# Optimization experiments

Measured on AMD Instinct MI355X. Metric: run time of the kernel, lower is better.

## Reference

```python
import jax, jax.numpy as jnp
import numpy as np

N_USERS = 50000
N_ITEMS = 30000
N_ENT = 100000
N_REL = 11          # relations are 1..10; table has N_REL-1 rows
E = 500000          # KG triplets
EI = 1000000        # user-item interaction edges
D = 64              # emb_size (must equal 2*KD for router input)
KD = 32             # FactSemanticEmbedding embedding_dim (complex half-dim)
HID = 64            # GatingRouter hidden (channel)
HOPS = 3            # context_hops
NTH = 3             # hop_threshold N
GAMMA = 0.2


def setup_inputs() -> dict:
    key = jax.random.key(0)
    ks = jax.random.split(key, 24)
    g = lambda i, shape, s=0.1: (jax.random.normal(ks[i], shape) * s).astype(jnp.float32)
    return dict(
        user_embed=g(0, (N_USERS, D)), item_embed=g(1, (N_ITEMS, D)),
        Wq=g(2, (D, D)), Wk=g(3, (D, D)), Wv=g(4, (D, D)),
        ent_real=g(5, (N_ENT, KD)), ent_imag=g(6, (N_ENT, KD)),
        rel_real=g(7, (N_REL - 1, KD)), rel_imag=g(8, (N_REL - 1, KD)),
        fp_W1=g(9, (6 * KD, 2 * KD)), fp_b1=jnp.zeros((2 * KD,), jnp.float32),
        fp_W2=g(10, (2 * KD, 3)), fp_b2=jnp.zeros((3,), jnp.float32),
        rt_W1=g(11, (D, HID)), rt_b1=jnp.zeros((HID,), jnp.float32),
        rt_W2=g(12, (HID, D)), rt_b2=jnp.zeros((D,), jnp.float32),
        relation_emb=g(13, (N_REL - 1, D)),
        user_emb=g(14, (N_USERS, D)), entity_emb=g(15, (N_ENT, D)),
        inter_edge_w=jax.random.uniform(ks[16], (EI,), jnp.float32),
        edge_index=jax.random.randint(ks[17], (2, E), 0, N_ENT),
        edge_type=jax.random.randint(ks[18], (E,), 1, N_REL),
        inter_edge=jnp.stack([jax.random.randint(ks[19], (EI,), 0, N_USERS),
                              jax.random.randint(ks[20], (EI,), 0, N_ITEMS)]),
    )


def _normalize(x):  # F.normalize(dim=-1, eps=1e-8)
    n = jnp.linalg.norm(x, axis=-1, keepdims=True)
    return x / jnp.maximum(n, 1e-8)


def _n2n(x):
    return jnp.nan_to_num(x, nan=0.0, posinf=1e4, neginf=1e-4)


def reference(user_embed, item_embed, Wq, Wk, Wv, ent_real, ent_imag, rel_real,
              rel_imag, fp_W1, fp_b1, fp_W2, fp_b2, rt_W1, rt_b1, rt_W2, rt_b2,
              relation_emb, user_emb, entity_emb, inter_edge_w,
              edge_index, edge_type, inter_edge):
    users, items = inter_edge[0], inter_edge[1]
    # --- AttentionPreferenceMiner (dropout off / eval) ---
    q = (user_embed @ Wq)[users]           # [EI, D]
    k = (item_embed @ Wk)[items]
    v = (item_embed @ Wv)[items]
    scores = (q * k).sum(-1) / jnp.sqrt(jnp.float32(D)) * inter_edge_w
    m = jax.ops.segment_max(scores, users, num_segments=N_USERS)
    ex = jnp.exp(scores - m[users])
    den = jax.ops.segment_sum(ex, users, num_segments=N_USERS)
    alpha = ex / den[users]                # scatter_softmax over users
    cnt_u = jax.ops.segment_sum(jnp.ones_like(scores), users, num_segments=N_USERS)
    user_pref = jax.ops.segment_sum(v * alpha[:, None], users, num_segments=N_USERS)
    user_pref = user_pref / jnp.maximum(cnt_u, 1.0)[:, None]   # scatter_mean
    # --- FactSemanticEmbedding ---
    h, t = edge_index[0], edge_index[1]
    r = edge_type - 1
    hr, hi = ent_real[h], ent_imag[h]
    rr, ri = rel_real[r], rel_imag[r]
    tr, ti = ent_real[t], ent_imag[t]
    feat = jnp.concatenate([hr, hi, rr, ri, tr, ti], axis=-1)  # [E, 6*KD]
    w = jax.nn.softmax(jax.nn.sigmoid(feat @ fp_W1 + fp_b1) @ fp_W2 + fp_b2, axis=-1)
    br = w[:, 0:1] * hr + w[:, 1:2] * rr + w[:, 2:3] * tr
    bi = w[:, 0:1] * hi + w[:, 1:2] * ri + w[:, 2:3] * ti
    fact = jnp.concatenate([br, bi], axis=1)                   # [E, D]
    # --- GatingRouter: sum_j (aligned @ pref^T)[i,j] == aligned @ pref.sum(0) ---
    aligned = jax.nn.sigmoid(fact @ rt_W1 + rt_b1) @ rt_W2 + rt_b2
    omega = (aligned @ user_pref.sum(0)) / jnp.sqrt(jnp.float32(HID))  # [E]
    # --- GraphConv (mess_dropout off) ---
    rel_e = relation_emb[r]                                    # [E, D]
    cnt_h = jax.ops.segment_sum(jnp.ones((E,), omega.dtype), h, num_segments=N_ENT)
    seg_o = jax.ops.segment_sum(omega, h, num_segments=E)      # dim_size=omega.shape[0]
    alpha_g = omega / (seg_o[h] + 1e-8)
    eta = jnp.where(alpha_g > GAMMA, alpha_g, 0.0)
    seg_e = jax.ops.segment_sum(eta, h, num_segments=E)
    eta = eta / (seg_e[h] + 1e-8)
    e_emb, u_emb = entity_emb, user_emb
    ent_res, usr_res = entity_emb, user_emb
    for hop in range(1, HOPS + 1):
        neigh = e_emb[t] * rel_e
        rho = alpha_g if hop < NTH else eta
        e_agg = jax.ops.segment_sum(rho[:, None] * neigh, h, num_segments=N_ENT)
        e_agg = e_agg / jnp.maximum(cnt_h, 1.0)[:, None]       # scatter_mean
        item_agg = inter_edge_w[:, None] * e_emb[items]
        u_agg = jax.ops.segment_sum(item_agg, users, num_segments=N_USERS)
        e_emb = _n2n(_normalize(e_agg))
        u_emb = _n2n(_normalize(u_agg))
        ent_res = ent_res + e_emb
        usr_res = usr_res + u_emb
    return jnp.concatenate([ent_res, usr_res], axis=0)        # [N_ENT+N_USERS, D]
```

## Files before the change

### kernel.cpp

```cpp
#include <hip/hip_runtime.h>
#include <hip/hip_bf16.h>
#include <math.h>

#define N_USERS 50000
#define N_ITEMS 30000
#define N_ENT   100000
#define NE      500000
#define NEI     1000000
#define D       64
#define GAMMA   0.2f
#define LDP     65

#define UBK ((N_USERS + 255) / 256)
#define HBK ((N_ENT + 255) / 256)
#define PCHUNK 4096

typedef __hip_bfloat16 bf16;

__device__ __forceinline__ float wave_sum(float v) {
    #pragma unroll
    for (int off = 32; off > 0; off >>= 1) v += __shfl_xor(v, off, 64);
    return v;
}

__device__ __forceinline__ float g16_sum(float v) {
    #pragma unroll
    for (int off = 1; off < 16; off <<= 1) v += __shfl_xor(v, off, 64);
    return v;
}

__device__ __forceinline__ float bits2f(unsigned short u) {
    return __uint_as_float(((unsigned)u) << 16);
}

__device__ __forceinline__ unsigned short f2bf_bits(float f) {
    bf16 b = __float2bfloat16(f);
    return *(unsigned short*)&b;
}

__device__ __forceinline__ float sigmoidf(float x) {
    return __fdividef(1.0f, 1.0f + __expf(-x));
}

__device__ __forceinline__ float n2n(float y) {
    if (isnan(y)) return 0.0f;
    if (isinf(y)) return y > 0.0f ? 1e4f : 1e-4f;
    return y;
}

__global__ __launch_bounds__(256) void k_histb(const int* __restrict__ ie,
        const int* __restrict__ eidx, int* __restrict__ bcntU,
        int* __restrict__ bcntH, int UCH) {
    __shared__ int lc[HBK + 1];
    int t = threadIdx.x;
    int b = blockIdx.x;
    for (int i = t; i < HBK + 1; i += 256) lc[i] = 0;
    __syncthreads();
    if (b < UCH) {
        int base = b * PCHUNK;
        #pragma unroll
        for (int i = 0; i < PCHUNK / 256; i++) {
            int e = base + i * 256 + t;
            if (e < NEI) atomicAdd(&lc[ie[e] >> 8], 1);
        }
        __syncthreads();
        for (int i = t; i < UBK; i += 256) if (lc[i]) atomicAdd(&bcntU[i], lc[i]);
    } else {
        int base = (b - UCH) * PCHUNK;
        #pragma unroll
        for (int i = 0; i < PCHUNK / 256; i++) {
            int e = base + i * 256 + t;
            if (e < NE) atomicAdd(&lc[eidx[e] >> 8], 1);
        }
        __syncthreads();
        for (int i = t; i < HBK; i += 256) if (lc[i]) atomicAdd(&bcntH[i], lc[i]);
    }
}

__global__ void k_scanb(const int* __restrict__ bcntU, int* __restrict__ bOffU,
                        int* __restrict__ bcurU, const int* __restrict__ bcntH,
                        int* __restrict__ bOffH, int* __restrict__ bcurH,
                        int* __restrict__ offU, int* __restrict__ offH) {
    __shared__ int sh[512];
    int t = threadIdx.x;
    const int* c; int* o; int* cu; int n; int tot;
    if (blockIdx.x == 0) { c = bcntU; o = bOffU; cu = bcurU; n = UBK; tot = NEI; }
    else                 { c = bcntH; o = bOffH; cu = bcurH; n = HBK; tot = NE; }
    int v = (t < n) ? c[t] : 0;
    sh[t] = v;
    __syncthreads();
    for (int d = 1; d < 512; d <<= 1) {
        int x = (t >= d) ? sh[t - d] : 0;
        __syncthreads();
        sh[t] += x;
        __syncthreads();
    }
    if (t < n) { int ex = sh[t] - v; o[t] = ex; cu[t] = ex; }
    if (t == 0) {
        o[n] = tot;
        if (blockIdx.x == 0) offU[N_USERS] = NEI;
        else                 offH[N_ENT] = NE;
    }
}

__global__ __launch_bounds__(256) void k_part1(const int* __restrict__ ie,
        const float* __restrict__ w, const int* __restrict__ eidx,
        const int* __restrict__ etype, int* __restrict__ bcurU,
        int* __restrict__ bcurH, int2* __restrict__ stIW,
        int* __restrict__ stTR, int UCH) {
    __shared__ int lcnt[HBK + 1];
    __shared__ int lbase[HBK + 1];
    int t = threadIdx.x;
    int b = blockIdx.x;
    for (int i = t; i < HBK + 1; i += 256) lcnt[i] = 0;
    __syncthreads();
    if (b < UCH) {
        int base = b * PCHUNK;
        int bkt[PCHUNK / 256], rnk[PCHUNK / 256];
        #pragma unroll
        for (int i = 0; i < PCHUNK / 256; i++) {
            int e = base + i * 256 + t;
            bkt[i] = -1;
            rnk[i] = 0;
            if (e < NEI) {
                int k = ie[e] >> 8;
                bkt[i] = k;
                rnk[i] = atomicAdd(&lcnt[k], 1);
            }
        }
        __syncthreads();
        for (int i = t; i < UBK; i += 256)
            if (lcnt[i] > 0) lbase[i] = atomicAdd(&bcurU[i], lcnt[i]);
        __syncthreads();
        #pragma unroll
        for (int i = 0; i < PCHUNK / 256; i++) {
            int e = base + i * 256 + t;
            if (bkt[i] >= 0) {
                int pos = lbase[bkt[i]] + rnk[i];
                int ul = ie[e] & 255;
                stIW[pos] = make_int2(ie[NEI + e] | (ul << 24), __float_as_int(w[e]));
            }
        }
    } else {
        int base = (b - UCH) * PCHUNK;
        int bkt[PCHUNK / 256], rnk[PCHUNK / 256];
        #pragma unroll
        for (int i = 0; i < PCHUNK / 256; i++) {
            int e = base + i * 256 + t;
            bkt[i] = -1;
            rnk[i] = 0;
            if (e < NE) {
                int k = eidx[e] >> 8;
                bkt[i] = k;
                rnk[i] = atomicAdd(&lcnt[k], 1);
            }
        }
        __syncthreads();
        for (int i = t; i < HBK; i += 256)
            if (lcnt[i] > 0) lbase[i] = atomicAdd(&bcurH[i], lcnt[i]);
        __syncthreads();
        #pragma unroll
        for (int i = 0; i < PCHUNK / 256; i++) {
            int e = base + i * 256 + t;
            if (bkt[i] >= 0) {
                int pos = lbase[bkt[i]] + rnk[i];
                int hl = eidx[e] & 255;
                stTR[pos] = eidx[NE + e] | ((etype[e] - 1) << 20) | (hl << 24);
            }
        }
    }
}

__global__ __launch_bounds__(256) void k_part2(const int* __restrict__ bOffU,
        const int2* __restrict__ stIW, int* __restrict__ offU,
        int2* __restrict__ csr_itw, const int* __restrict__ bOffH,
        const int* __restrict__ stTR, int* __restrict__ offH,
        int2* __restrict__ csr_th, int UBKc) {
    __shared__ int lcnt[256];
    __shared__ int lcur[256];
    int t = threadIdx.x;
    int b = blockIdx.x;
    lcnt[t] = 0;
    __syncthreads();
    if (b < UBKc) {
        int s = bOffU[b], e = bOffU[b + 1];
        for (int j = s + t; j < e; j += 256)
            atomicAdd(&lcnt[((unsigned)stIW[j].x) >> 24], 1);
        __syncthreads();
        int v = lcnt[t];
        lcur[t] = v;
        __syncthreads();
        for (int d = 1; d < 256; d <<= 1) {
            int x = (t >= d) ? lcur[t - d] : 0;
            __syncthreads();
            lcur[t] += x;
            __syncthreads();
        }
        int base = s + lcur[t] - v;
        int u = (b << 8) + t;
        if (u < N_USERS) offU[u] = base;
        __syncthreads();
        lcur[t] = base;
        __syncthreads();
        for (int j = s + t; j < e; j += 256) {
            int2 r = stIW[j];
            int pos = atomicAdd(&lcur[((unsigned)r.x) >> 24], 1);
            csr_itw[pos] = make_int2(r.x & 0x00FFFFFF, r.y);
        }
    } else {
        int bb = b - UBKc;
        int s = bOffH[bb], e = bOffH[bb + 1];
        for (int j = s + t; j < e; j += 256)
            atomicAdd(&lcnt[((unsigned)stTR[j]) >> 24], 1);
        __syncthreads();
        int v = lcnt[t];
        lcur[t] = v;
        __syncthreads();
        for (int d = 1; d < 256; d <<= 1) {
            int x = (t >= d) ? lcur[t - d] : 0;
            __syncthreads();
            lcur[t] += x;
            __syncthreads();
        }
        int base = s + lcur[t] - v;
        int h = (bb << 8) + t;
        if (h < N_ENT) offH[h] = base;
        __syncthreads();
        lcur[t] = base;
        __syncthreads();
        for (int j = s + t; j < e; j += 256) {
            int r = stTR[j];
            int pos = atomicAdd(&lcur[((unsigned)r) >> 24], 1);
            csr_th[pos] = make_int2(r & 0x00FFFFFF,
                                    (bb << 8) + (int)(((unsigned)r) >> 24));
        }
    }
}

__device__ __forceinline__ void stage_rows2(const float* __restrict__ s0,
                                            const float* __restrict__ s1,
                                            float* At, int row0, int n, int t) {
    #pragma unroll
    for (int half = 0; half < 2; half++) {
        const float* src = half ? s1 : s0;
        int kofs = half ? 32 : 0;
        #pragma unroll
        for (int fi = t, it = 0; it < 2; fi += 256, it++) {
            int row = fi >> 3;
            int k4 = (fi & 7) << 2;
            float4 v = make_float4(0.f, 0.f, 0.f, 0.f);
            if (row0 + row < n) v = *(const float4*)&src[(size_t)(row0 + row) * 32 + k4];
            At[(kofs + k4 + 0) * LDP + row] = v.x;
            At[(kofs + k4 + 1) * LDP + row] = v.y;
            At[(kofs + k4 + 2) * LDP + row] = v.z;
            At[(kofs + k4 + 3) * LDP + row] = v.w;
        }
    }
}

__device__ __forceinline__ void stage_rows1(const float* __restrict__ src,
                                            float* At, int row0, int n, int t) {
    #pragma unroll
    for (int fi = t, it = 0; it < 4; fi += 256, it++) {
        int row = fi >> 4;
        int k4 = (fi & 15) << 2;
        float4 v = make_float4(0.f, 0.f, 0.f, 0.f);
        if (row0 + row < n) v = *(const float4*)&src[(size_t)(row0 + row) * 64 + k4];
        At[(k4 + 0) * LDP + row] = v.x;
        At[(k4 + 1) * LDP + row] = v.y;
        At[(k4 + 2) * LDP + row] = v.z;
        At[(k4 + 3) * LDP + row] = v.w;
    }
}

__global__ __launch_bounds__(256) void k_proj(const float* __restrict__ I,
        const float* __restrict__ Wk, const float* __restrict__ Wv,
        const float* __restrict__ UE, const float* __restrict__ Wq,
        bf16* __restrict__ IkB, float* __restrict__ Iv, float* __restrict__ Uq, int IB) {
    __shared__ float At[64 * LDP];
    int t = threadIdx.x;
    int b = blockIdx.x;
    int lane = t & 63;
    int wv = __builtin_amdgcn_readfirstlane(t >> 6);
    if (b < IB) {
        int row0 = b << 6;
        stage_rows1(I, At, row0, N_ITEMS, t);
        __syncthreads();
        const float* Wb = ((wv >> 1) ? Wv : Wk) + (wv & 1) * 32;
        float acc[32];
        #pragma unroll
        for (int c = 0; c < 32; c++) acc[c] = 0.f;
        for (int k = 0; k < 64; k++) {
            float a = At[k * LDP + lane];
            const float* wr = Wb + k * 64;
            #pragma unroll
            for (int c4 = 0; c4 < 8; c4++) {
                float4 w4 = *(const float4*)&wr[c4 * 4];
                acc[c4 * 4 + 0] += a * w4.x;
                acc[c4 * 4 + 1] += a * w4.y;
                acc[c4 * 4 + 2] += a * w4.z;
                acc[c4 * 4 + 3] += a * w4.w;
            }
        }
        int row = row0 + lane;
        if (row < N_ITEMS) {
            if (wv >> 1) {
                float* dst = Iv + (size_t)row * 64 + (wv & 1) * 32;
                #pragma unroll
                for (int c4 = 0; c4 < 8; c4++)
                    *(float4*)&dst[c4 * 4] = make_float4(acc[c4*4], acc[c4*4+1], acc[c4*4+2], acc[c4*4+3]);
            } else {
                bf16* dst = IkB + (size_t)row * 64 + (wv & 1) * 32;
                #pragma unroll
                for (int c4 = 0; c4 < 8; c4++) {
                    ushort4 s;
                    s.x = f2bf_bits(acc[c4 * 4 + 0]);
                    s.y = f2bf_bits(acc[c4 * 4 + 1]);
                    s.z = f2bf_bits(acc[c4 * 4 + 2]);
                    s.w = f2bf_bits(acc[c4 * 4 + 3]);
                    *(ushort4*)&dst[c4 * 4] = s;
                }
            }
        }
    } else {
        int row0 = (b - IB) << 6;
        stage_rows1(UE, At, row0, N_USERS, t);
        __syncthreads();
        const float* Wb = Wq + wv * 16;
        float acc[16];
        #pragma unroll
        for (int c = 0; c < 16; c++) acc[c] = 0.f;
        for (int k = 0; k < 64; k++) {
            float a = At[k * LDP + lane];
            const float* wr = Wb + k * 64;
            #pragma unroll
            for (int c4 = 0; c4 < 4; c4++) {
                float4 w4 = *(const float4*)&wr[c4 * 4];
                acc[c4 * 4 + 0] += a * w4.x;
                acc[c4 * 4 + 1] += a * w4.y;
                acc[c4 * 4 + 2] += a * w4.z;
                acc[c4 * 4 + 3] += a * w4.w;
            }
        }
        int row = row0 + lane;
        if (row < N_USERS) {
            float* dst = Uq + (size_t)row * 64 + wv * 16;
            #pragma unroll
            for (int c4 = 0; c4 < 4; c4++)
                *(float4*)&dst[c4 * 4] = make_float4(acc[c4*4], acc[c4*4+1], acc[c4*4+2], acc[c4*4+3]);
        }
    }
}

__global__ __launch_bounds__(256) void k_userAB(const int* __restrict__ offU,
                        const int2* __restrict__ itw,
                        const float* __restrict__ Uq, const bf16* __restrict__ IkB,
                        float* __restrict__ exA, float* __restrict__ c, int n) {
    int u = (blockIdx.x * blockDim.x + threadIdx.x) >> 6;
    int lane = threadIdx.x & 63;
    if (u >= n) return;
    int s = offU[u], e = offU[u + 1];
    if (s == e) return;
    int l = lane & 15, g = lane >> 4;
    float4 qv = *(const float4*)&Uq[(size_t)u * D + l * 4];
    const char* kbase = (const char*)IkB;
    unsigned dby = (unsigned)(l << 3);
    float den = 0.f;
    for (int j0 = s; j0 < e; j0 += 8) {
        int jA = j0 + g, jB = jA + 4;
        bool vA = jA < e, vB = jB < e;
        int2 iA = itw[vA ? jA : s];
        int2 iB = itw[vB ? jB : s];
        ushort4 kA = *(const ushort4*)(kbase + (((unsigned)iA.x) << 7) + dby);
        ushort4 kB = *(const ushort4*)(kbase + (((unsigned)iB.x) << 7) + dby);
        float dA = qv.x * bits2f(kA.x) + qv.y * bits2f(kA.y) +
                   qv.z * bits2f(kA.z) + qv.w * bits2f(kA.w);
        float dB = qv.x * bits2f(kB.x) + qv.y * bits2f(kB.y) +
                   qv.z * bits2f(kB.z) + qv.w * bits2f(kB.w);
        #pragma unroll
        for (int off = 1; off < 16; off <<= 1) {
            dA += __shfl_xor(dA, off, 64);
            dB += __shfl_xor(dB, off, 64);
        }
        float eAv = vA ? __expf(dA * 0.125f * __int_as_float(iA.y)) : 0.f;
        float eBv = vB ? __expf(dB * 0.125f * __int_as_float(iB.y)) : 0.f;
        den += eAv + eBv;
        if (vA && l == 0) exA[jA] = eAv;
        if (vB && l == 0) exA[jB] = eBv;
    }
    den += __shfl_xor(den, 16, 64);
    den += __shfl_xor(den, 32, 64);
    float inv = __fdividef(1.0f, den * (float)(e - s));
    asm volatile("s_waitcnt vmcnt(0)" ::: "memory");
    for (int j = s + lane; j < e; j += 64)
        atomicAdd(&c[itw[j].x], exA[j] * inv);
}

__global__ void k_pdense(const float* __restrict__ c, const float* __restrict__ Iv,
                         float* __restrict__ p, int n) {
    int lane = threadIdx.x & 63;
    int gw = blockIdx.x * 4 + (threadIdx.x >> 6);
    int nw = gridDim.x * 4;
    float acc = 0.f;
    for (int i = gw; i < n; i += nw) acc += c[i] * Iv[(size_t)i * D + lane];
    __shared__ float red[256];
    red[threadIdx.x] = acc;
    __syncthreads();
    if (threadIdx.x < 64) {
        float s = red[threadIdx.x] + red[threadIdx.x + 64] + red[threadIdx.x + 128] + red[threadIdx.x + 192];
        atomicAdd(&p[threadIdx.x], s);
    }
}

__global__ __launch_bounds__(256) void k_entabx(const float* __restrict__ er,
        const float* __restrict__ ei, const float* __restrict__ fpW1,
        const float* __restrict__ rr, const float* __restrict__ ri,
        const float* __restrict__ rtW1, const float* __restrict__ rtW2,
        const float* __restrict__ rt_b2, const float* __restrict__ p,
        float* __restrict__ EH, float* __restrict__ ET, float* __restrict__ PHI,
        float* __restrict__ RR1, float* __restrict__ PSI,
        float* __restrict__ v2, float* __restrict__ cb, int EB) {
    __shared__ float At[64 * LDP];
    int b = blockIdx.x;
    int t = threadIdx.x;
    if (b < EB) {
        int row0 = b << 6;
        stage_rows2(er, ei, At, row0, N_ENT, t);
        __syncthreads();
        int lane = t & 63;
        int wv = __builtin_amdgcn_readfirstlane(t >> 6);
        int row = row0 + lane;
        const float* Wb1 = fpW1 + ((wv >> 1) ? (128 * 64) : 0) + (wv & 1) * 32;
        const float* Wb2 = rtW1 + wv * 16;
        float acc[32];
        float acp[16];
        #pragma unroll
        for (int c = 0; c < 32; c++) acc[c] = 0.f;
        #pragma unroll
        for (int c = 0; c < 16; c++) acp[c] = 0.f;
        for (int k = 0; k < 64; k++) {
            float a = At[k * LDP + lane];
            const float* wr1 = Wb1 + k * 64;
            const float* wr2 = Wb2 + k * 64;
            #pragma unroll
            for (int c4 = 0; c4 < 8; c4++) {
                float4 w4 = *(const float4*)&wr1[c4 * 4];
                acc[c4 * 4 + 0] += a * w4.x;
                acc[c4 * 4 + 1] += a * w4.y;
                acc[c4 * 4 + 2] += a * w4.z;
                acc[c4 * 4 + 3] += a * w4.w;
            }
            #pragma unroll
            for (int c4 = 0; c4 < 4; c4++) {
                float4 w4 = *(const float4*)&wr2[c4 * 4];
                acp[c4 * 4 + 0] += a * w4.x;
                acp[c4 * 4 + 1] += a * w4.y;
                acp[c4 * 4 + 2] += a * w4.z;
                acp[c4 * 4 + 3] += a * w4.w;
            }
        }
        if (row < N_ENT) {
            float* dst = ((wv >> 1) ? ET : EH) + (size_t)row * 64 + (wv & 1) * 32;
            #pragma unroll
            for (int c4 = 0; c4 < 8; c4++)
                *(float4*)&dst[c4 * 4] = make_float4(acc[c4*4], acc[c4*4+1], acc[c4*4+2], acc[c4*4+3]);
            float* dsp = PHI + (size_t)row * 64 + wv * 16;
            #pragma unroll
            for (int c4 = 0; c4 < 4; c4++)
                *(float4*)&dsp[c4 * 4] = make_float4(acp[c4*4], acp[c4*4+1], acp[c4*4+2], acp[c4*4+3]);
        }
    } else if (b == EB) {
        if (t < 64) {
            int lane = t;
            for (int r = 0; r < 10; r++) {
                float a = 0.f, bb = 0.f;
                for (int k = 0; k < 32; k++) {
                    float sr = rr[r * 32 + k], si = ri[r * 32 + k];
                    a  += sr * fpW1[(64 + k) * D + lane] + si * fpW1[(96 + k) * D + lane];
                    bb += sr * rtW1[k * D + lane] + si * rtW1[(32 + k) * D + lane];
                }
                RR1[r * D + lane] = a;
                PSI[r * D + lane] = bb;
            }
        }
    } else {
        if (t < 64) {
            int j = t;
            float acc = 0.f;
            #pragma unroll
            for (int k = 0; k < D; k++) acc += rtW2[j * D + k] * p[k];
            v2[j] = acc;
            float cc = rt_b2[j] * p[j];
            cc = wave_sum(cc);
            if (j == 0) cb[0] = cc;
        }
    }
}

__global__ __launch_bounds__(256) void k_omegaE(const int2* __restrict__ csr_th,
                          const float* __restrict__ EH, const float* __restrict__ ET,
                          const float* __restrict__ PHI, const float* __restrict__ PSI,
                          const float* __restrict__ RR1, const float* __restrict__ fp_b1,
                          const float* __restrict__ fpW2, const float* __restrict__ fp_b2,
                          const float* __restrict__ rt_b1, const float* __restrict__ v2,
                          const float* __restrict__ cb, float* __restrict__ omg,
                          const float* __restrict__ src_emb, bf16* __restrict__ eA,
                          int NB) {
    int b = blockIdx.x;
    if (b >= NB) {
        int base = (b - NB) * 1024 + threadIdx.x * 4;
        float4 v = *(const float4*)&src_emb[base];
        ushort4 s;
        s.x = f2bf_bits(v.x); s.y = f2bf_bits(v.y);
        s.z = f2bf_bits(v.z); s.w = f2bf_bits(v.w);
        *(ushort4*)&eA[base] = s;
        return;
    }
    int grp = threadIdx.x >> 4;
    int l = threadIdx.x & 15;
    int d0 = l * 4;
    int jA = b * 32 + grp;
    int jB = jA + 16;
    float4 b1 = *(const float4*)&fp_b1[d0];
    float4 rb = *(const float4*)&rt_b1[d0];
    float4 vv = *(const float4*)&v2[d0];
    float cc = cb[0];
    float f0[4], f1[4], f2[4];
    #pragma unroll
    for (int c4 = 0; c4 < 4; c4++) {
        f0[c4] = fpW2[(d0 + c4) * 3 + 0];
        f1[c4] = fpW2[(d0 + c4) * 3 + 1];
        f2[c4] = fpW2[(d0 + c4) * 3 + 2];
    }
    float b20 = fp_b2[0], b21 = fp_b2[1], b22 = fp_b2[2];
    int2 thA = csr_th[jA];
    int2 thB = csr_th[jB];
    int tA = thA.x & 0xFFFFF, rA = thA.x >> 20, hA = thA.y;
    int tB = thB.x & 0xFFFFF, rB = thB.x >> 20, hB = thB.y;
    float4 ehA = *(const float4*)&EH[(size_t)hA * D + d0];
    float4 ehB = *(const float4*)&EH[(size_t)hB * D + d0];
    float4 phA = *(const float4*)&PHI[(size_t)hA * D + d0];
    float4 phB = *(const float4*)&PHI[(size_t)hB * D + d0];
    float4 etA = *(const float4*)&ET[(size_t)tA * D + d0];
    float4 etB = *(const float4*)&ET[(size_t)tB * D + d0];
    float4 ptA = *(const float4*)&PHI[(size_t)tA * D + d0];
    float4 ptB = *(const float4*)&PHI[(size_t)tB * D + d0];
    float4 rrA = *(const float4*)&RR1[rA * D + d0];
    float4 rrB = *(const float4*)&RR1[rB * D + d0];
    float4 psA = *(const float4*)&PSI[rA * D + d0];
    float4 psB = *(const float4*)&PSI[rB * D + d0];
    ehA.x += b1.x; ehA.y += b1.y; ehA.z += b1.z; ehA.w += b1.w;
    ehB.x += b1.x; ehB.y += b1.y; ehB.z += b1.z; ehB.w += b1.w;
    float zA0 = sigmoidf(ehA.x + rrA.x + etA.x);
    float zA1 = sigmoidf(ehA.y + rrA.y + etA.y);
    float zA2 = sigmoidf(ehA.z + rrA.z + etA.z);
    float zA3 = sigmoidf(ehA.w + rrA.w + etA.w);
    float zB0 = sigmoidf(ehB.x + rrB.x + etB.x);
    float zB1 = sigmoidf(ehB.y + rrB.y + etB.y);
    float zB2 = sigmoidf(ehB.z + rrB.z + etB.z);
    float zB3 = sigmoidf(ehB.w + rrB.w + etB.w);
    float v[6];
    v[0] = zA0 * f0[0] + zA1 * f0[1] + zA2 * f0[2] + zA3 * f0[3];
    v[1] = zA0 * f1[0] + zA1 * f1[1] + zA2 * f1[2] + zA3 * f1[3];
    v[2] = zA0 * f2[0] + zA1 * f2[1] + zA2 * f2[2] + zA3 * f2[3];
    v[3] = zB0 * f0[0] + zB1 * f0[1] + zB2 * f0[2] + zB3 * f0[3];
    v[4] = zB0 * f1[0] + zB1 * f1[1] + zB2 * f1[2] + zB3 * f1[3];
    v[5] = zB0 * f2[0] + zB1 * f2[1] + zB2 * f2[2] + zB3 * f2[3];
    #pragma unroll
    for (int off = 1; off < 16; off <<= 1) {
        #pragma unroll
        for (int q = 0; q < 6; q++) v[q] += __shfl_xor(v[q], off, 64);
    }
    float a0 = v[0] + b20, a1 = v[1] + b21, a2 = v[2] + b22;
    float mx = fmaxf(a0, fmaxf(a1, a2));
    float e0 = __expf(a0 - mx), e1 = __expf(a1 - mx), e2 = __expf(a2 - mx);
    float isum = __fdividef(1.0f, e0 + e1 + e2);
    float WA0 = e0 * isum, WA1 = e1 * isum, WA2 = e2 * isum;
    a0 = v[3] + b20; a1 = v[4] + b21; a2 = v[5] + b22;
    mx = fmaxf(a0, fmaxf(a1, a2));
    e0 = __expf(a0 - mx); e1 = __expf(a1 - mx); e2 = __expf(a2 - mx);
    isum = __fdividef(1.0f, e0 + e1 + e2);
    float WB0 = e0 * isum, WB1 = e1 * isum, WB2 = e2 * isum;
    float svA = sigmoidf(WA0 * phA.x + WA1 * psA.x + WA2 * ptA.x + rb.x) * vv.x
              + sigmoidf(WA0 * phA.y + WA1 * psA.y + WA2 * ptA.y + rb.y) * vv.y
              + sigmoidf(WA0 * phA.z + WA1 * psA.z + WA2 * ptA.z + rb.z) * vv.z
              + sigmoidf(WA0 * phA.w + WA1 * psA.w + WA2 * ptA.w + rb.w) * vv.w;
    float svB = sigmoidf(WB0 * phB.x + WB1 * psB.x + WB2 * ptB.x + rb.x) * vv.x
              + sigmoidf(WB0 * phB.y + WB1 * psB.y + WB2 * ptB.y + rb.y) * vv.y
              + sigmoidf(WB0 * phB.z + WB1 * psB.z + WB2 * ptB.z + rb.z) * vv.z
              + sigmoidf(WB0 * phB.w + WB1 * psB.w + WB2 * ptB.w + rb.w) * vv.w;
    #pragma unroll
    for (int off = 1; off < 16; off <<= 1) {
        svA += __shfl_xor(svA, off, 64);
        svB += __shfl_xor(svB, off, 64);
    }
    if (l == 0) {
        omg[jA] = (svA + cc) * 0.125f;
        omg[jB] = (svB + cc) * 0.125f;
    }
}

__global__ __launch_bounds__(256) void k_omegaS(const int* __restrict__ offH,
                          const int2* __restrict__ csr_th,
                          const float* __restrict__ omg,
                          int2* __restrict__ pa, int2* __restrict__ pe, int n) {
    int h = (blockIdx.x * 256 + threadIdx.x) >> 4;
    int l = threadIdx.x & 15;
    if (h >= n) return;
    int s = offH[h], e = offH[h + 1];
    if (s == e) return;
    float so = 0.f;
    for (int j = s + l; j < e; j += 16) so += omg[j];
    so = g16_sum(so);
    float invO = __fdividef(1.0f, so + 1e-8f);
    float se = 0.f;
    for (int j = s + l; j < e; j += 16) {
        float a = omg[j] * invO;
        pa[j] = make_int2(csr_th[j].x, __float_as_int(a));
        se += (a > GAMMA) ? a : 0.0f;
    }
    se = g16_sum(se);
    float invE = __fdividef(1.0f, se + 1e-8f);
    for (int j = s + l; j < e; j += 16) {
        float a = omg[j] * invO;
        pe[j] = make_int2(csr_th[j].x, __float_as_int(((a > GAMMA) ? a : 0.0f) * invE));
    }
}

__global__ __launch_bounds__(256) void k_hop(const int* __restrict__ offH,
                      const int2* __restrict__ rt,
                      const float* __restrict__ rel,
                      const int* __restrict__ offU, const int2* __restrict__ itw,
                      const bf16* __restrict__ ecur, bf16* __restrict__ enxt,
                      const float* __restrict__ initE, const float* __restrict__ initU,
                      float* __restrict__ outE, float* __restrict__ outU,
                      int init, int EB2) {
    int b = blockIdx.x;
    int l = threadIdx.x & 15;
    int d0 = l * 4;
    const char* ebase = (const char*)ecur;
    unsigned dby = (unsigned)(d0 << 1);
    if (b < EB2) {
        int gw = (b * 256 + threadIdx.x) >> 4;
        if (gw >= N_ENT) return;
        int s = offH[gw], e = offH[gw + 1];
        float a0 = 0.f, a1 = 0.f, a2 = 0.f, a3 = 0.f;
        for (int j0 = s; j0 < e; j0 += 2) {
            int jB = j0 + 1;
            bool vB = jB < e;
            int2 pA = rt[j0];
            int2 pB = rt[vB ? jB : j0];
            float rhA = __int_as_float(pA.y);
            float rhB = vB ? __int_as_float(pB.y) : 0.f;
            unsigned tA = (unsigned)pA.x & 0xFFFFFu; int rA = pA.x >> 20;
            unsigned tB = (unsigned)pB.x & 0xFFFFFu; int rB = pB.x >> 20;
            ushort4 evA = *(const ushort4*)(ebase + (tA << 7) + dby);
            ushort4 evB = *(const ushort4*)(ebase + (tB << 7) + dby);
            float4 rlA = *(const float4*)&rel[rA * D + d0];
            float4 rlB = *(const float4*)&rel[rB * D + d0];
            a0 += rhA * bits2f(evA.x) * rlA.x;
            a1 += rhA * bits2f(evA.y) * rlA.y;
            a2 += rhA * bits2f(evA.z) * rlA.z;
            a3 += rhA * bits2f(evA.w) * rlA.w;
            a0 += rhB * bits2f(evB.x) * rlB.x;
            a1 += rhB * bits2f(evB.y) * rlB.y;
            a2 += rhB * bits2f(evB.z) * rlB.z;
            a3 += rhB * bits2f(evB.w) * rlB.w;
        }
        float invd = __fdividef(1.0f, fmaxf((float)(e - s), 1.0f));
        a0 *= invd; a1 *= invd; a2 *= invd; a3 *= invd;
        float ss = a0 * a0 + a1 * a1 + a2 * a2 + a3 * a3;
        ss = g16_sum(ss);
        float nrm = fmaxf(sqrtf(ss), 1e-8f);
        float innrm = __fdividef(1.0f, nrm);
        float y0 = n2n(a0 * innrm), y1 = n2n(a1 * innrm), y2 = n2n(a2 * innrm), y3 = n2n(a3 * innrm);
        ushort4 st;
        st.x = f2bf_bits(y0); st.y = f2bf_bits(y1); st.z = f2bf_bits(y2); st.w = f2bf_bits(y3);
        *(ushort4*)&enxt[(size_t)gw * D + d0] = st;
        size_t o = (size_t)gw * D + d0;
        float4 prev;
        if (init) prev = *(const float4*)&initE[o];
        else      prev = *(const float4*)&outE[o];
        *(float4*)&outE[o] = make_float4(prev.x + y0, prev.y + y1, prev.z + y2, prev.w + y3);
    } else {
        int gw = ((b - EB2) * 256 + threadIdx.x) >> 4;
        if (gw >= N_USERS) return;
        int s = offU[gw], e = offU[gw + 1];
        float a0 = 0.f, a1 = 0.f, a2 = 0.f, a3 = 0.f;
        for (int j0 = s; j0 < e; j0 += 2) {
            int jB = j0 + 1;
            bool vB = jB < e;
            int2 iA = itw[j0];
            int2 iB = itw[vB ? jB : j0];
            float wA = __int_as_float(iA.y);
            float wB = vB ? __int_as_float(iB.y) : 0.f;
            ushort4 evA = *(const ushort4*)(ebase + (((unsigned)iA.x) << 7) + dby);
            ushort4 evB = *(const ushort4*)(ebase + (((unsigned)iB.x) << 7) + dby);
            a0 += wA * bits2f(evA.x) + wB * bits2f(evB.x);
            a1 += wA * bits2f(evA.y) + wB * bits2f(evB.y);
            a2 += wA * bits2f(evA.z) + wB * bits2f(evB.z);
            a3 += wA * bits2f(evA.w) + wB * bits2f(evB.w);
        }
        float ss = a0 * a0 + a1 * a1 + a2 * a2 + a3 * a3;
        ss = g16_sum(ss);
        float nrm = fmaxf(sqrtf(ss), 1e-8f);
        float innrm = __fdividef(1.0f, nrm);
        float y0 = n2n(a0 * innrm), y1 = n2n(a1 * innrm), y2 = n2n(a2 * innrm), y3 = n2n(a3 * innrm);
        size_t o = (size_t)gw * D + d0;
        float4 prev;
        if (init) prev = *(const float4*)&initU[o];
        else      prev = *(const float4*)&outU[o];
        *(float4*)&outU[o] = make_float4(prev.x + y0, prev.y + y1, prev.z + y2, prev.w + y3);
    }
}

extern "C" void kernel_launch(void* const* d_in, const int* in_sizes, int n_in,
                              void* d_out, int out_size, void* d_ws, size_t ws_size,
                              hipStream_t stream) {
    const float* user_embed = (const float*)d_in[0];
    const float* item_embed = (const float*)d_in[1];
    const float* Wq = (const float*)d_in[2];
    const float* Wk = (const float*)d_in[3];
    const float* Wv = (const float*)d_in[4];
    const float* ent_real = (const float*)d_in[5];
    const float* ent_imag = (const float*)d_in[6];
    const float* rel_real = (const float*)d_in[7];
    const float* rel_imag = (const float*)d_in[8];
    const float* fp_W1 = (const float*)d_in[9];
    const float* fp_b1 = (const float*)d_in[10];
    const float* fp_W2 = (const float*)d_in[11];
    const float* fp_b2 = (const float*)d_in[12];
    const float* rt_W1 = (const float*)d_in[13];
    const float* rt_b1 = (const float*)d_in[14];
    const float* rt_W2 = (const float*)d_in[15];
    const float* rt_b2 = (const float*)d_in[16];
    const float* relation_emb = (const float*)d_in[17];
    const float* user_emb = (const float*)d_in[18];
    const float* entity_emb = (const float*)d_in[19];
    const float* inter_edge_w = (const float*)d_in[20];
    const int* edge_index = (const int*)d_in[21];
    const int* edge_type = (const int*)d_in[22];
    const int* inter_edge = (const int*)d_in[23];
    float* out = (float*)d_out;

    float* W = (float*)d_ws;
    size_t off = 0;
    auto alloc = [&](size_t n) { float* r = W + off; off += n; return r; };
    float* omg    = alloc(NE);
    float* exA    = alloc(NEI);
    float* c      = alloc(N_ITEMS);
    float* p      = alloc(64);
    float* v2     = alloc(64);
    float* cb     = alloc(64);
    float* RR1    = alloc(10 * D);
    float* PSI    = alloc(10 * D);
    off = (off + 3) & ~(size_t)3;
    int* IW = (int*)(W + off);
    size_t ioff = 0;
    auto ialloc = [&](size_t n) { int* r = IW + ioff; ioff += n; return r; };
    int2* csr_itw = (int2*)ialloc(2 * (size_t)NEI);
    int2* pa      = (int2*)ialloc(2 * (size_t)NE);
    int2* pe      = (int2*)ialloc(2 * (size_t)NE);
    int2* csr_th  = (int2*)ialloc(2 * (size_t)NE);
    int* offU   = ialloc(N_USERS + 1);
    int* offH   = ialloc(N_ENT + 1);
    int* bcntU  = ialloc(UBK);
    int* bcntH  = ialloc(HBK);
    int* bOffU  = ialloc(UBK + 1);
    int* bOffH  = ialloc(HBK + 1);
    int* bcurU  = ialloc(UBK);
    int* bcurH  = ialloc(HBK);
    off += ioff;
    off = (off + 3) & ~(size_t)3;
    float* U = W + off;
    int2* stIW = (int2*)U;
    int*  stTR = (int*)U + 2 * (size_t)NEI;
    bf16*  IkB = (bf16*)U;
    float* Iv  = U + (size_t)N_ITEMS * 32;
    float* Uq  = Iv + (size_t)N_ITEMS * D;
    float* EH  = U;
    float* ET  = U + (size_t)N_ENT * D;
    float* PHI = U + 2 * (size_t)N_ENT * D;
    bf16*  eA  = (bf16*)(U + 3 * (size_t)N_ENT * D);
    bf16* eB = (bf16*)U;

    const int UCH = (NEI + PCHUNK - 1) / PCHUNK;
    const int HCH = (NE + PCHUNK - 1) / PCHUNK;
    const int IB = (N_ITEMS + 63) / 64;
    const int UB = (N_USERS + 63) / 64;
    const int EB = (N_ENT + 63) / 64;
    const int OEB = NE / 32;
    const int CB = (N_ENT * D) / 1024;
    const int SB = (N_ENT + 15) / 16;
    const int HE2 = (N_ENT + 15) / 16;
    const int HU2 = (N_USERS + 15) / 16;

    hipMemsetAsync(bcntU, 0, (UBK + HBK) * 4, stream);
    hipMemsetAsync(c, 0, (N_ITEMS + 64) * 4, stream);
    k_histb<<<UCH + HCH, 256, 0, stream>>>(inter_edge, edge_index, bcntU, bcntH, UCH);
    k_scanb<<<2, 512, 0, stream>>>(bcntU, bOffU, bcurU, bcntH, bOffH, bcurH, offU, offH);
    k_part1<<<UCH + HCH, 256, 0, stream>>>(inter_edge, inter_edge_w, edge_index,
                                           edge_type, bcurU, bcurH, stIW, stTR, UCH);
    k_part2<<<UBK + HBK, 256, 0, stream>>>(bOffU, stIW, offU, csr_itw,
                                           bOffH, stTR, offH, csr_th, UBK);

    k_proj<<<IB + UB, 256, 0, stream>>>(item_embed, Wk, Wv, user_embed, Wq,
                                        IkB, Iv, Uq, IB);
    k_userAB<<<(N_USERS + 3) / 4, 256, 0, stream>>>(offU, csr_itw, Uq, IkB, exA, c, N_USERS);
    k_pdense<<<64, 256, 0, stream>>>(c, Iv, p, N_ITEMS);

    k_entabx<<<EB + 2, 256, 0, stream>>>(ent_real, ent_imag, fp_W1, rel_real, rel_imag,
                                         rt_W1, rt_W2, rt_b2, p, EH, ET, PHI,
                                         RR1, PSI, v2, cb, EB);
    k_omegaE<<<OEB + CB, 256, 0, stream>>>(csr_th, EH, ET, PHI, PSI, RR1,
                                           fp_b1, fp_W2, fp_b2, rt_b1, v2, cb,
                                           omg, entity_emb, eA, OEB);
    k_omegaS<<<SB, 256, 0, stream>>>(offH, csr_th, omg, pa, pe, N_ENT);

    bf16* ecur = eA;
    bf16* enxt = eB;
    for (int hop = 1; hop <= 3; hop++) {
        const int2* rt = (hop < 3) ? pa : pe;
        int init = (hop == 1) ? 1 : 0;
        k_hop<<<HE2 + HU2, 256, 0, stream>>>(offH, rt, relation_emb,
                                             offU, csr_itw, ecur, enxt,
                                             entity_emb, user_emb,
                                             out, out + (size_t)N_ENT * D, init, HE2);
        bf16* tmp = ecur; ecur = enxt; enxt = tmp;
    }
}
```

Before: 642.7 us.

## Fuse entity projection into item/user projection kernel, split out v2 tiny kernel

Moves the entity-side GEMMs (EH/ET/PHI) and relation tables (RR1/PSI) out of k_entabx and into the front projection kernel, interleaving entity blocks with item/user blocks in one launch. The small p-dependent v2/cb computation becomes its own single-block kernel after k_pdense. Workspace is relaid so the item/user projection buffers no longer alias EH/ET/PHI. This aims to fill the GPU better during the earlier projection phase and leave only a tiny kernel on the p-dependent path, at the cost of a larger workspace footprint.

```diff
diff --git a/kernel.cpp b/kernel.cpp
--- a/kernel.cpp
+++ b/kernel.cpp
@@ -273,17 +273,70 @@
     }
 }
 
-__global__ __launch_bounds__(256) void k_proj(const float* __restrict__ I,
+__global__ __launch_bounds__(256) void k_front(const float* __restrict__ I,
         const float* __restrict__ Wk, const float* __restrict__ Wv,
         const float* __restrict__ UE, const float* __restrict__ Wq,
-        bf16* __restrict__ IkB, float* __restrict__ Iv, float* __restrict__ Uq, int IB) {
+        bf16* __restrict__ IkB, float* __restrict__ Iv, float* __restrict__ Uq,
+        const float* __restrict__ er, const float* __restrict__ ei,
+        const float* __restrict__ fpW1, const float* __restrict__ rr,
+        const float* __restrict__ ri, const float* __restrict__ rtW1,
+        float* __restrict__ EH, float* __restrict__ ET, float* __restrict__ PHI,
+        float* __restrict__ RR1, float* __restrict__ PSI, int IB, int UB, int EB) {
     __shared__ float At[64 * LDP];
+    int b = blockIdx.x;
     int t = threadIdx.x;
-    int b = blockIdx.x;
+    int OTH = IB + UB + 1;
+    int role, idx;
+    if (b < 2 * OTH) { role = b & 1; idx = b >> 1; }
+    else             { role = 1;     idx = OTH + (b - 2 * OTH); }
     int lane = t & 63;
     int wv = __builtin_amdgcn_readfirstlane(t >> 6);
-    if (b < IB) {
-        int row0 = b << 6;
+    if (role == 1) {
+        int row0 = idx << 6;
+        stage_rows2(er, ei, At, row0, N_ENT, t);
+        __syncthreads();
+        int row = row0 + lane;
+        const float* Wb1 = fpW1 + ((wv >> 1) ? (128 * 64) : 0) + (wv & 1) * 32;
+        const float* Wb2 = rtW1 + wv * 16;
+        float acc[32];
+        float acp[16];
+        #pragma unroll
+        for (int c = 0; c < 32; c++) acc[c] = 0.f;
+        #pragma unroll
+        for (int c = 0; c < 16; c++) acp[c] = 0.f;
+        for (int k = 0; k < 64; k++) {
+            float a = At[k * LDP + lane];
+            const float* wr1 = Wb1 + k * 64;
+            const float* wr2 = Wb2 + k * 64;
+            #pragma unroll
+            for (int c4 = 0; c4 < 8; c4++) {
+                float4 w4 = *(const float4*)&wr1[c4 * 4];
+                acc[c4 * 4 + 0] += a * w4.x;
+                acc[c4 * 4 + 1] += a * w4.y;
+                acc[c4 * 4 + 2] += a * w4.z;
+                acc[c4 * 4 + 3] += a * w4.w;
+            }
+            #pragma unroll
+            for (int c4 = 0; c4 < 4; c4++) {
+                float4 w4 = *(const float4*)&wr2[c4 * 4];
+                acp[c4 * 4 + 0] += a * w4.x;
+                acp[c4 * 4 + 1] += a * w4.y;
+                acp[c4 * 4 + 2] += a * w4.z;
+                acp[c4 * 4 + 3] += a * w4.w;
+            }
+        }
+        if (row < N_ENT) {
+            float* dst = ((wv >> 1) ? ET : EH) + (size_t)row * 64 + (wv & 1) * 32;
+            #pragma unroll
+            for (int c4 = 0; c4 < 8; c4++)
+                *(float4*)&dst[c4 * 4] = make_float4(acc[c4*4], acc[c4*4+1], acc[c4*4+2], acc[c4*4+3]);
+            float* dsp = PHI + (size_t)row * 64 + wv * 16;
+            #pragma unroll
+            for (int c4 = 0; c4 < 4; c4++)
+                *(float4*)&dsp[c4 * 4] = make_float4(acp[c4*4], acp[c4*4+1], acp[c4*4+2], acp[c4*4+3]);
+        }
+    } else if (idx < IB) {
+        int row0 = idx << 6;
         stage_rows1(I, At, row0, N_ITEMS, t);
         __syncthreads();
         const float* Wb = ((wv >> 1) ? Wv : Wk) + (wv & 1) * 32;
@@ -322,8 +375,8 @@
                 }
             }
         }
-    } else {
-        int row0 = (b - IB) << 6;
+    } else if (idx < IB + UB) {
+        int row0 = (idx - IB) << 6;
         stage_rows1(UE, At, row0, N_USERS, t);
         __syncthreads();
         const float* Wb = Wq + wv * 16;
@@ -348,6 +401,20 @@
             #pragma unroll
             for (int c4 = 0; c4 < 4; c4++)
                 *(float4*)&dst[c4 * 4] = make_float4(acc[c4*4], acc[c4*4+1], acc[c4*4+2], acc[c4*4+3]);
+        }
+    } else {
+        if (t < 64) {
+            int lane2 = t;
+            for (int r = 0; r < 10; r++) {
+                float a = 0.f, bb = 0.f;
+                for (int k = 0; k < 32; k++) {
+                    float sr = rr[r * 32 + k], si = ri[r * 32 + k];
+                    a  += sr * fpW1[(64 + k) * D + lane2] + si * fpW1[(96 + k) * D + lane2];
+                    bb += sr * rtW1[k * D + lane2] + si * rtW1[(32 + k) * D + lane2];
+                }
+                RR1[r * D + lane2] = a;
+                PSI[r * D + lane2] = bb;
+            }
         }
     }
 }
@@ -412,88 +479,18 @@
     }
 }
 
-__global__ __launch_bounds__(256) void k_entabx(const float* __restrict__ er,
-        const float* __restrict__ ei, const float* __restrict__ fpW1,
-        const float* __restrict__ rr, const float* __restrict__ ri,
-        const float* __restrict__ rtW1, const float* __restrict__ rtW2,
-        const float* __restrict__ rt_b2, const float* __restrict__ p,
-        float* __restrict__ EH, float* __restrict__ ET, float* __restrict__ PHI,
-        float* __restrict__ RR1, float* __restrict__ PSI,
-        float* __restrict__ v2, float* __restrict__ cb, int EB) {
-    __shared__ float At[64 * LDP];
-    int b = blockIdx.x;
-    int t = threadIdx.x;
-    if (b < EB) {
-        int row0 = b << 6;
-        stage_rows2(er, ei, At, row0, N_ENT, t);
-        __syncthreads();
-        int lane = t & 63;
-        int wv = __builtin_amdgcn_readfirstlane(t >> 6);
-        int row = row0 + lane;
-        const float* Wb1 = fpW1 + ((wv >> 1) ? (128 * 64) : 0) + (wv & 1) * 32;
-        const float* Wb2 = rtW1 + wv * 16;
-        float acc[32];
-        float acp[16];
-        #pragma unroll
-        for (int c = 0; c < 32; c++) acc[c] = 0.f;
-        #pragma unroll
-        for (int c = 0; c < 16; c++) acp[c] = 0.f;
-        for (int k = 0; k < 64; k++) {
-            float a = At[k * LDP + lane];
-            const float* wr1 = Wb1 + k * 64;
-            const float* wr2 = Wb2 + k * 64;
-            #pragma unroll
-            for (int c4 = 0; c4 < 8; c4++) {
-                float4 w4 = *(const float4*)&wr1[c4 * 4];
-                acc[c4 * 4 + 0] += a * w4.x;
-                acc[c4 * 4 + 1] += a * w4.y;
-                acc[c4 * 4 + 2] += a * w4.z;
-                acc[c4 * 4 + 3] += a * w4.w;
-            }
-            #pragma unroll
-            for (int c4 = 0; c4 < 4; c4++) {
-                float4 w4 = *(const float4*)&wr2[c4 * 4];
-                acp[c4 * 4 + 0] += a * w4.x;
-                acp[c4 * 4 + 1] += a * w4.y;
-                acp[c4 * 4 + 2] += a * w4.z;
-                acp[c4 * 4 + 3] += a * w4.w;
-            }
-        }
-        if (row < N_ENT) {
-            float* dst = ((wv >> 1) ? ET : EH) + (size_t)row * 64 + (wv & 1) * 32;
-            #pragma unroll
-            for (int c4 = 0; c4 < 8; c4++)
-                *(float4*)&dst[c4 * 4] = make_float4(acc[c4*4], acc[c4*4+1], acc[c4*4+2], acc[c4*4+3]);
-            float* dsp = PHI + (size_t)row * 64 + wv * 16;
-            #pragma unroll
-            for (int c4 = 0; c4 < 4; c4++)
-                *(float4*)&dsp[c4 * 4] = make_float4(acp[c4*4], acp[c4*4+1], acp[c4*4+2], acp[c4*4+3]);
-        }
-    } else if (b == EB) {
-        if (t < 64) {
-            int lane = t;
-            for (int r = 0; r < 10; r++) {
-                float a = 0.f, bb = 0.f;
-                for (int k = 0; k < 32; k++) {
-                    float sr = rr[r * 32 + k], si = ri[r * 32 + k];
-                    a  += sr * fpW1[(64 + k) * D + lane] + si * fpW1[(96 + k) * D + lane];
-                    bb += sr * rtW1[k * D + lane] + si * rtW1[(32 + k) * D + lane];
-                }
-                RR1[r * D + lane] = a;
-                PSI[r * D + lane] = bb;
-            }
-        }
-    } else {
-        if (t < 64) {
-            int j = t;
-            float acc = 0.f;
-            #pragma unroll
-            for (int k = 0; k < D; k++) acc += rtW2[j * D + k] * p[k];
-            v2[j] = acc;
-            float cc = rt_b2[j] * p[j];
-            cc = wave_sum(cc);
-            if (j == 0) cb[0] = cc;
-        }
+__global__ void k_v2(const float* __restrict__ rtW2, const float* __restrict__ rt_b2,
+                     const float* __restrict__ p, float* __restrict__ v2,
+                     float* __restrict__ cb) {
+    int j = threadIdx.x;
+    if (j < 64) {
+        float acc = 0.f;
+        #pragma unroll
+        for (int k = 0; k < D; k++) acc += rtW2[j * D + k] * p[k];
+        v2[j] = acc;
+        float cc = rt_b2[j] * p[j];
+        cc = wave_sum(cc);
+        if (j == 0) cb[0] = cc;
     }
 }
 
@@ -773,15 +770,17 @@
     off += ioff;
     off = (off + 3) & ~(size_t)3;
     float* U = W + off;
+    const size_t NED = (size_t)N_ENT * D;
     int2* stIW = (int2*)U;
     int*  stTR = (int*)U + 2 * (size_t)NEI;
-    bf16*  IkB = (bf16*)U;
-    float* Iv  = U + (size_t)N_ITEMS * 32;
+    float* EH  = U;
+    float* ET  = U + NED;
+    float* PHI = U + 2 * NED;
+    float* XR  = U + 3 * NED;
+    bf16*  IkB = (bf16*)XR;
+    float* Iv  = XR + (size_t)N_ITEMS * 32;
     float* Uq  = Iv + (size_t)N_ITEMS * D;
-    float* EH  = U;
-    float* ET  = U + (size_t)N_ENT * D;
-    float* PHI = U + 2 * (size_t)N_ENT * D;
-    bf16*  eA  = (bf16*)(U + 3 * (size_t)N_ENT * D);
+    bf16* eA = (bf16*)XR;
     bf16* eB = (bf16*)U;
 
     const int UCH = (NEI + PCHUNK - 1) / PCHUNK;
@@ -789,6 +788,7 @@
     const int IB = (N_ITEMS + 63) / 64;
     const int UB = (N_USERS + 63) / 64;
     const int EB = (N_ENT + 63) / 64;
+    const int OTH = IB + UB + 1;
     const int OEB = NE / 32;
     const int CB = (N_ENT * D) / 1024;
     const int SB = (N_ENT + 15) / 16;
@@ -804,14 +804,16 @@
     k_part2<<<UBK + HBK, 256, 0, stream>>>(bOffU, stIW, offU, csr_itw,
                                            bOffH, stTR, offH, csr_th, UBK);
 
-    k_proj<<<IB + UB, 256, 0, stream>>>(item_embed, Wk, Wv, user_embed, Wq,
-                                        IkB, Iv, Uq, IB);
+    k_front<<<OTH + EB, 256, 0, stream>>>(item_embed, Wk, Wv, user_embed, Wq,
+                                          IkB, Iv, Uq,
+                                          ent_real, ent_imag, fp_W1,
+                                          rel_real, rel_imag, rt_W1,
+                                          EH, ET, PHI, RR1, PSI, IB, UB, EB);
+
     k_userAB<<<(N_USERS + 3) / 4, 256, 0, stream>>>(offU, csr_itw, Uq, IkB, exA, c, N_USERS);
     k_pdense<<<64, 256, 0, stream>>>(c, Iv, p, N_ITEMS);
-
-    k_entabx<<<EB + 2, 256, 0, stream>>>(ent_real, ent_imag, fp_W1, rel_real, rel_imag,
-                                         rt_W1, rt_W2, rt_b2, p, EH, ET, PHI,
-                                         RR1, PSI, v2, cb, EB);
+    k_v2<<<1, 64, 0, stream>>>(rt_W2, rt_b2, p, v2, cb);
+
     k_omegaE<<<OEB + CB, 256, 0, stream>>>(csr_th, EH, ET, PHI, PSI, RR1,
                                            fp_b1, fp_W2, fp_b2, rt_b1, v2, cb,
                                            omg, entity_emb, eA, OEB);
```

Measured after the change: 645.0 us. Within noise of the previous version (+0.4%).

## Unroll user aggregation gather by four and separate workspace buffers

Applied to the files above, without the earlier changes.

The user-side weighted gather loop now loads four interaction entries and four entity rows per iteration instead of two. This gives each thread more memory loads in flight to hide gather latency. The workspace layout is also changed so the item attention buffers (IkB/Iv/Uq) and eA sit beyond the EH/ET/PHI region instead of aliasing it. That may let stages that were serialised by buffer reuse overlap, or it may be a correctness fix, at the cost of a larger workspace footprint.

```diff
diff --git a/kernel.cpp b/kernel.cpp
--- a/kernel.cpp
+++ b/kernel.cpp
@@ -687,19 +687,25 @@
         if (gw >= N_USERS) return;
         int s = offU[gw], e = offU[gw + 1];
         float a0 = 0.f, a1 = 0.f, a2 = 0.f, a3 = 0.f;
-        for (int j0 = s; j0 < e; j0 += 2) {
-            int jB = j0 + 1;
-            bool vB = jB < e;
-            int2 iA = itw[j0];
-            int2 iB = itw[vB ? jB : j0];
-            float wA = __int_as_float(iA.y);
-            float wB = vB ? __int_as_float(iB.y) : 0.f;
-            ushort4 evA = *(const ushort4*)(ebase + (((unsigned)iA.x) << 7) + dby);
-            ushort4 evB = *(const ushort4*)(ebase + (((unsigned)iB.x) << 7) + dby);
-            a0 += wA * bits2f(evA.x) + wB * bits2f(evB.x);
-            a1 += wA * bits2f(evA.y) + wB * bits2f(evB.y);
-            a2 += wA * bits2f(evA.z) + wB * bits2f(evB.z);
-            a3 += wA * bits2f(evA.w) + wB * bits2f(evB.w);
+        for (int j0 = s; j0 < e; j0 += 4) {
+            int j1 = j0 + 1, j2 = j0 + 2, j3 = j0 + 3;
+            bool v1 = j1 < e, v2c = j2 < e, v3 = j3 < e;
+            int2 i0 = itw[j0];
+            int2 i1 = itw[v1 ? j1 : j0];
+            int2 i2 = itw[v2c ? j2 : j0];
+            int2 i3 = itw[v3 ? j3 : j0];
+            float w0 = __int_as_float(i0.y);
+            float w1 = v1 ? __int_as_float(i1.y) : 0.f;
+            float w2 = v2c ? __int_as_float(i2.y) : 0.f;
+            float w3 = v3 ? __int_as_float(i3.y) : 0.f;
+            ushort4 e0 = *(const ushort4*)(ebase + (((unsigned)i0.x) << 7) + dby);
+            ushort4 e1 = *(const ushort4*)(ebase + (((unsigned)i1.x) << 7) + dby);
+            ushort4 e2 = *(const ushort4*)(ebase + (((unsigned)i2.x) << 7) + dby);
+            ushort4 e3 = *(const ushort4*)(ebase + (((unsigned)i3.x) << 7) + dby);
+            a0 += w0 * bits2f(e0.x) + w1 * bits2f(e1.x) + w2 * bits2f(e2.x) + w3 * bits2f(e3.x);
+            a1 += w0 * bits2f(e0.y) + w1 * bits2f(e1.y) + w2 * bits2f(e2.y) + w3 * bits2f(e3.y);
+            a2 += w0 * bits2f(e0.z) + w1 * bits2f(e1.z) + w2 * bits2f(e2.z) + w3 * bits2f(e3.z);
+            a3 += w0 * bits2f(e0.w) + w1 * bits2f(e1.w) + w2 * bits2f(e2.w) + w3 * bits2f(e3.w);
         }
         float ss = a0 * a0 + a1 * a1 + a2 * a2 + a3 * a3;
         ss = g16_sum(ss);
@@ -773,15 +779,17 @@
     off += ioff;
     off = (off + 3) & ~(size_t)3;
     float* U = W + off;
+    const size_t NED = (size_t)N_ENT * D;
     int2* stIW = (int2*)U;
     int*  stTR = (int*)U + 2 * (size_t)NEI;
-    bf16*  IkB = (bf16*)U;
-    float* Iv  = U + (size_t)N_ITEMS * 32;
+    float* EH  = U;
+    float* ET  = U + NED;
+    float* PHI = U + 2 * NED;
+    float* XR  = U + 3 * NED;
+    bf16*  IkB = (bf16*)XR;
+    float* Iv  = XR + (size_t)N_ITEMS * 32;
     float* Uq  = Iv + (size_t)N_ITEMS * D;
-    float* EH  = U;
-    float* ET  = U + (size_t)N_ENT * D;
-    float* PHI = U + 2 * (size_t)N_ENT * D;
-    bf16*  eA  = (bf16*)(U + 3 * (size_t)N_ENT * D);
+    bf16* eA = (bf16*)XR;
     bf16* eB = (bf16*)U;
 
     const int UCH = (NEI + PCHUNK - 1) / PCHUNK;
```

Measured after the change: 629.6 us. -2.1%, faster.
